# Kernel optimization log

Measured on AMD Instinct MI355X. Metric: run time of the kernel, lower is better.

Reference implementation:

```python
import jax, jax.numpy as jnp
import numpy as np

V, E, H, S = 50257, 1024, 1024, 2048


def setup_inputs() -> dict:
    key = jax.random.key(0)
    ks = jax.random.split(key, 24)
    def n(k, shape, s=0.02):
        return jax.random.normal(k, shape, dtype=jnp.float32) * s
    inp = {
        "x": jax.random.normal(ks[0], (1, E), dtype=jnp.float32),
        "encoder_outputs": jax.random.normal(ks[1], (S, 2 * H), dtype=jnp.float32),
        "sentence": jax.random.randint(ks[2], (S,), 0, V, dtype=jnp.int32).at[0].set(7),
        "prev_probs": jax.random.uniform(ks[3], (V + S,), dtype=jnp.float32),
        "h0": n(ks[4], (1, H), 1.0),
        "c0": n(ks[5], (1, H), 1.0),
        "attn_W": n(ks[6], (S, 2 * H)), "attn_b": jnp.zeros((S,), jnp.float32),
        "comb_W": n(ks[7], (H, 2 * H)), "comb_b": jnp.zeros((H,), jnp.float32),
        "Ws_W": n(ks[8], (H, 2 * H)), "Ws_b": jnp.zeros((H,), jnp.float32),
        "Wo_W": n(ks[9], (V, H)), "Wo_b": jnp.zeros((V,), jnp.float32),
        "Wc_W": n(ks[10], (H, 2 * H)), "Wc_b": jnp.zeros((H,), jnp.float32),
        "W_ih": n(ks[11], (4 * H, E + 2 * H)), "W_hh": n(ks[12], (4 * H, H)),
        "b_ih": jnp.zeros((4 * H,), jnp.float32), "b_hh": jnp.zeros((4 * H,), jnp.float32),
        "prev_word": 7,
    }
    return inp


def reference(x, encoder_outputs, sentence, prev_probs, h0, c0,
              attn_W, attn_b, comb_W, comb_b, Ws_W, Ws_b,
              Wo_W, Wo_b, Wc_W, Wc_b, W_ih, W_hh, b_ih, b_hh, prev_word):
    xe, h, c = x[0], h0[0], c0[0]            # [E], [H], [H]
    # attentive read: attention over encoder positions, then combine to [H]
    att_logits = jnp.concatenate([xe, h]) @ attn_W.T + attn_b      # [S]
    attn_w = jax.nn.softmax(att_logits)
    ctx = attn_w @ encoder_outputs                                 # [2H]
    attentive = ctx @ comb_W.T + comb_b                            # [H]
    # selective read (copy mechanism): positions where sentence == prev_word
    probs_c = prev_probs[V:]                                       # [S]
    rho = jnp.where(sentence == prev_word, probs_c, 0.0)
    rho = rho / (rho.sum() + 1e-9)
    selective = (rho @ encoder_outputs) @ Ws_W.T + Ws_b            # [H]
    # single LSTM step (PyTorch gate order i,f,g,o)
    lstm_in = jnp.concatenate([xe, selective, attentive])          # [E+2H]
    gates = lstm_in @ W_ih.T + b_ih + h @ W_hh.T + b_hh            # [4H]
    i, f, g, o = jnp.split(gates, 4)
    c1 = jax.nn.sigmoid(f) * c + jax.nn.sigmoid(i) * jnp.tanh(g)
    h1 = jax.nn.sigmoid(o) * jnp.tanh(c1)                          # [H]
    # generate + copy scores, joint softmax
    score_g = h1 @ Wo_W.T + Wo_b                                   # [V]
    score_c = jnp.tanh(encoder_outputs @ Wc_W.T + Wc_b) @ h1       # [S]
    probs = jax.nn.softmax(jnp.concatenate([score_g, score_c]))    # [V+S]
    return probs, h1[None, :], c1[None, :]
```

## Files before the change

### kernel.cpp

```cpp
#include <hip/hip_runtime.h>
#include <hip/hip_bf16.h>
#include <math.h>

#define VV 50257
#define EE 1024
#define HH 1024
#define SS 2048
#define VS (VV + SS)

#define OFF_LOGA   0
#define OFF_ATTW   2048
#define OFF_RHO    4096
#define OFF_CTX    6144
#define OFF_SEL    8192
#define OFF_LSTMIN 10240
#define OFF_GATES  13312
#define OFF_H1     17408
#define OFF_LOG    18432
#define OFF_MS     70784
#define OFF_LS     70912
#define OFF_G      71040
#define OFF_TT     71168

typedef __attribute__((ext_vector_type(8))) short bf16x8;
typedef __attribute__((ext_vector_type(4))) float f32x4;

__device__ inline float wave_reduce(float v) {
    #pragma unroll
    for (int off = 32; off > 0; off >>= 1) v += __shfl_down(v, off, 64);
    return v;
}

__device__ inline unsigned short f2bf(float f) {
    unsigned int u = __builtin_bit_cast(unsigned int, f);
    u += 0x7FFFu + ((u >> 16) & 1u);
    return (unsigned short)(u >> 16);
}

__global__ void k_attn_logits(const float* __restrict__ x, const float* __restrict__ h0,
                              const float* __restrict__ attn_W, const float* __restrict__ attn_b,
                              float* __restrict__ out) {
    int wave = (blockIdx.x * blockDim.x + threadIdx.x) >> 6;
    int lane = threadIdx.x & 63;
    if (wave >= SS) return;
    const float4* rp = (const float4*)(attn_W + (size_t)wave * 2048);
    float acc = 0.f;
    #pragma unroll
    for (int k = 0; k < 8; ++k) {
        int idx = lane + 64 * k;
        float4 w = rp[idx];
        int j = idx * 4;
        const float* cat = (j < 1024) ? (x + j) : (h0 + (j - 1024));
        acc += w.x * cat[0] + w.y * cat[1] + w.z * cat[2] + w.w * cat[3];
    }
    acc = wave_reduce(acc);
    if (lane == 0) out[wave] = acc + attn_b[wave];
}

__global__ void k_prep(const float* __restrict__ logits, const int* __restrict__ sentence,
                       const float* __restrict__ prev_probs, const int* __restrict__ prev_word,
                       const float* __restrict__ x,
                       float* __restrict__ attn_w, float* __restrict__ rho,
                       float* __restrict__ lstm_in) {
    __shared__ float red[256];
    int tid = threadIdx.x;
    float m = -1e30f;
    for (int s = tid; s < SS; s += 256) m = fmaxf(m, logits[s]);
    red[tid] = m; __syncthreads();
    for (int o = 128; o > 0; o >>= 1) { if (tid < o) red[tid] = fmaxf(red[tid], red[tid + o]); __syncthreads(); }
    m = red[0]; __syncthreads();
    float sum = 0.f;
    for (int s = tid; s < SS; s += 256) sum += expf(logits[s] - m);
    red[tid] = sum; __syncthreads();
    for (int o = 128; o > 0; o >>= 1) { if (tid < o) red[tid] += red[tid + o]; __syncthreads(); }
    float inv = 1.f / red[0]; __syncthreads();
    for (int s = tid; s < SS; s += 256) attn_w[s] = expf(logits[s] - m) * inv;
    int pw = prev_word[0];
    float rsum = 0.f;
    for (int s = tid; s < SS; s += 256) rsum += (sentence[s] == pw) ? prev_probs[VV + s] : 0.f;
    red[tid] = rsum; __syncthreads();
    for (int o = 128; o > 0; o >>= 1) { if (tid < o) red[tid] += red[tid + o]; __syncthreads(); }
    float rinv = 1.f / (red[0] + 1e-9f); __syncthreads();
    for (int s = tid; s < SS; s += 256) rho[s] = ((sentence[s] == pw) ? prev_probs[VV + s] : 0.f) * rinv;
    for (int j = tid; j < EE; j += 256) lstm_in[j] = x[j];
}

__global__ void k_ctx(const float* __restrict__ enc, const float* __restrict__ attn_w,
                      const float* __restrict__ rho, float* __restrict__ ctx,
                      float* __restrict__ selctx) {
    int col = blockIdx.x * 256 + threadIdx.x;
    int s0 = blockIdx.y * 64;
    float a = 0.f, r = 0.f;
    const float* p = enc + (size_t)s0 * 2048 + col;
    #pragma unroll 4
    for (int i = 0; i < 64; ++i) {
        float v = p[(size_t)i * 2048];
        a += attn_w[s0 + i] * v;
        r += rho[s0 + i] * v;
    }
    atomicAdd(&ctx[col], a);
    atomicAdd(&selctx[col], r);
}

__global__ void k_comb(const float* __restrict__ ctx, const float* __restrict__ selctx,
                       const float* __restrict__ comb_W, const float* __restrict__ comb_b,
                       const float* __restrict__ Ws_W, const float* __restrict__ Ws_b,
                       float* __restrict__ lstm_in) {
    int wave = (blockIdx.x * blockDim.x + threadIdx.x) >> 6;
    int lane = threadIdx.x & 63;
    if (wave >= 2048) return;
    bool sel = wave >= 1024;
    int i = sel ? wave - 1024 : wave;
    const float4* rp = (const float4*)((sel ? Ws_W : comb_W) + (size_t)i * 2048);
    const float4* vp = (const float4*)(sel ? selctx : ctx);
    float acc = 0.f;
    #pragma unroll
    for (int k = 0; k < 8; ++k) {
        int idx = lane + 64 * k;
        float4 w = rp[idx]; float4 v = vp[idx];
        acc += w.x * v.x + w.y * v.y + w.z * v.z + w.w * v.w;
    }
    acc = wave_reduce(acc);
    if (lane == 0) lstm_in[sel ? (1024 + i) : (2048 + i)] = acc + (sel ? Ws_b[i] : comb_b[i]);
}

__global__ void k_gates(const float* __restrict__ lstm_in, const float* __restrict__ h0,
                        const float* __restrict__ W_ih, const float* __restrict__ W_hh,
                        const float* __restrict__ b_ih, const float* __restrict__ b_hh,
                        float* __restrict__ gates) {
    int wave = (blockIdx.x * blockDim.x + threadIdx.x) >> 6;
    int lane = threadIdx.x & 63;
    if (wave >= 4096) return;
    const float4* rp = (const float4*)(W_ih + (size_t)wave * 3072);
    const float4* vp = (const float4*)lstm_in;
    float acc = 0.f;
    #pragma unroll
    for (int k = 0; k < 12; ++k) {
        int idx = lane + 64 * k;
        float4 w = rp[idx]; float4 v = vp[idx];
        acc += w.x * v.x + w.y * v.y + w.z * v.z + w.w * v.w;
    }
    const float4* hp = (const float4*)(W_hh + (size_t)wave * 1024);
    const float4* h4 = (const float4*)h0;
    #pragma unroll
    for (int k = 0; k < 4; ++k) {
        int idx = lane + 64 * k;
        float4 w = hp[idx]; float4 v = h4[idx];
        acc += w.x * v.x + w.y * v.y + w.z * v.z + w.w * v.w;
    }
    acc = wave_reduce(acc);
    if (lane == 0) gates[wave] = acc + b_ih[wave] + b_hh[wave];
}

__global__ void k_lstm(const float* __restrict__ gates, const float* __restrict__ c0,
                       float* __restrict__ out, float* __restrict__ h1ws) {
    int k = blockIdx.x * 256 + threadIdx.x;
    float ig = gates[k], fg = gates[1024 + k], gg = gates[2048 + k], og = gates[3072 + k];
    float si = 1.f / (1.f + expf(-ig));
    float sf = 1.f / (1.f + expf(-fg));
    float so = 1.f / (1.f + expf(-og));
    float c1 = sf * c0[k] + si * tanhf(gg);
    float h1 = so * tanhf(c1);
    out[VS + k] = h1;
    out[VS + 1024 + k] = c1;
    h1ws[k] = h1;
}

__global__ __launch_bounds__(256) void k_wc_gemm(const float* __restrict__ A,
                                                 const float* __restrict__ B,
                                                 const float* __restrict__ bias,
                                                 float* __restrict__ C) {
    __shared__ unsigned short As[128 * 32];
    __shared__ unsigned short Bs[128 * 32];
    int tid = threadIdx.x;
    int mbase = blockIdx.y * 128;
    int nbase = blockIdx.x * 128;
    int lane = tid & 63;
    int wid = tid >> 6;
    int wm = (wid >> 1) * 64;
    int wn = (wid & 1) * 64;
    int lrow = lane & 15;
    int lk = (lane >> 4) * 8;
    f32x4 acc[4][4] = {};
    for (int k0 = 0; k0 < 2048; k0 += 32) {
        #pragma unroll
        for (int i = 0; i < 4; ++i) {
            int fi = tid + 256 * i;
            int row = fi >> 3;
            int kg = fi & 7;
            float4 v = *(const float4*)(A + (size_t)(mbase + row) * 2048 + k0 + kg * 4);
            ushort4 a4 = { f2bf(v.x), f2bf(v.y), f2bf(v.z), f2bf(v.w) };
            *(ushort4*)(As + row * 32 + kg * 4) = a4;
            float4 w = *(const float4*)(B + (size_t)(nbase + row) * 2048 + k0 + kg * 4);
            ushort4 b4 = { f2bf(w.x), f2bf(w.y), f2bf(w.z), f2bf(w.w) };
            *(ushort4*)(Bs + row * 32 + kg * 4) = b4;
        }
        __syncthreads();
        bf16x8 af[4], bfr[4];
        #pragma unroll
        for (int t = 0; t < 4; ++t) {
            af[t]  = *(const bf16x8*)(As + (wm + t * 16 + lrow) * 32 + lk);
            bfr[t] = *(const bf16x8*)(Bs + (wn + t * 16 + lrow) * 32 + lk);
        }
        #pragma unroll
        for (int mt = 0; mt < 4; ++mt)
            #pragma unroll
            for (int nt = 0; nt < 4; ++nt)
                acc[mt][nt] = __builtin_amdgcn_mfma_f32_16x16x32_bf16(af[mt], bfr[nt], acc[mt][nt], 0, 0, 0);
        __syncthreads();
    }
    int crow0 = (lane >> 4) * 4;
    int ccol = lane & 15;
    #pragma unroll
    for (int mt = 0; mt < 4; ++mt)
        #pragma unroll
        for (int nt = 0; nt < 4; ++nt) {
            int col = nbase + wn + nt * 16 + ccol;
            float bb = bias[col];
            #pragma unroll
            for (int r = 0; r < 4; ++r) {
                int row = mbase + wm + mt * 16 + crow0 + r;
                C[(size_t)row * 1024 + col] = tanhf(acc[mt][nt][r] + bb);
            }
        }
}

__global__ void k_scores(const float* __restrict__ Wo_W, const float* __restrict__ Wo_b,
                         const float* __restrict__ Tt, const float* __restrict__ h1,
                         float* __restrict__ logits) {
    int wave = (blockIdx.x * blockDim.x + threadIdx.x) >> 6;
    int lane = threadIdx.x & 63;
    if (wave >= VS) return;
    const float* row = (wave < VV) ? (Wo_W + (size_t)wave * 1024) : (Tt + (size_t)(wave - VV) * 1024);
    const float4* rp = (const float4*)row;
    const float4* hp = (const float4*)h1;
    float acc = 0.f;
    #pragma unroll
    for (int k = 0; k < 4; ++k) {
        int idx = lane + 64 * k;
        float4 w = rp[idx]; float4 v = hp[idx];
        acc += w.x * v.x + w.y * v.y + w.z * v.z + w.w * v.w;
    }
    acc = wave_reduce(acc);
    if (lane == 0) logits[wave] = acc + (wave < VV ? Wo_b[wave] : 0.f);
}

__global__ void k_sm1(const float* __restrict__ logits, float* __restrict__ ms, float* __restrict__ ls) {
    __shared__ float rm[256], rl[256];
    int tid = threadIdx.x;
    float m = -1e30f, l = 0.f;
    for (int v = blockIdx.x * 256 + tid; v < VS; v += 128 * 256) {
        float x = logits[v];
        float nm = fmaxf(m, x);
        l = l * expf(m - nm) + expf(x - nm);
        m = nm;
    }
    rm[tid] = m; rl[tid] = l; __syncthreads();
    for (int o = 128; o > 0; o >>= 1) {
        if (tid < o) {
            float m2 = rm[tid + o], l2 = rl[tid + o];
            float nm = fmaxf(rm[tid], m2);
            rl[tid] = rl[tid] * expf(rm[tid] - nm) + l2 * expf(m2 - nm);
            rm[tid] = nm;
        }
        __syncthreads();
    }
    if (tid == 0) { ms[blockIdx.x] = rm[0]; ls[blockIdx.x] = rl[0]; }
}

__global__ void k_sm2(const float* __restrict__ ms, const float* __restrict__ ls, float* __restrict__ g) {
    __shared__ float rm[128], rl[128];
    int tid = threadIdx.x;
    rm[tid] = ms[tid]; rl[tid] = ls[tid]; __syncthreads();
    for (int o = 64; o > 0; o >>= 1) {
        if (tid < o) {
            float m2 = rm[tid + o], l2 = rl[tid + o];
            float nm = fmaxf(rm[tid], m2);
            rl[tid] = rl[tid] * expf(rm[tid] - nm) + l2 * expf(m2 - nm);
            rm[tid] = nm;
        }
        __syncthreads();
    }
    if (tid == 0) { g[0] = rm[0]; g[1] = 1.f / rl[0]; }
}

__global__ void k_sm3(const float* __restrict__ logits, const float* __restrict__ g,
                      float* __restrict__ out) {
    int v = blockIdx.x * 256 + threadIdx.x;
    if (v < VS) out[v] = expf(logits[v] - g[0]) * g[1];
}

extern "C" void kernel_launch(void* const* d_in, const int* in_sizes, int n_in,
                              void* d_out, int out_size, void* d_ws, size_t ws_size,
                              hipStream_t stream) {
    (void)in_sizes; (void)n_in; (void)out_size; (void)ws_size;
    const float* x          = (const float*)d_in[0];
    const float* enc        = (const float*)d_in[1];
    const int*   sentence   = (const int*)d_in[2];
    const float* prev_probs = (const float*)d_in[3];
    const float* h0         = (const float*)d_in[4];
    const float* c0         = (const float*)d_in[5];
    const float* attn_W     = (const float*)d_in[6];
    const float* attn_b     = (const float*)d_in[7];
    const float* comb_W     = (const float*)d_in[8];
    const float* comb_b     = (const float*)d_in[9];
    const float* Ws_W       = (const float*)d_in[10];
    const float* Ws_b       = (const float*)d_in[11];
    const float* Wo_W       = (const float*)d_in[12];
    const float* Wo_b       = (const float*)d_in[13];
    const float* Wc_W       = (const float*)d_in[14];
    const float* Wc_b       = (const float*)d_in[15];
    const float* W_ih       = (const float*)d_in[16];
    const float* W_hh       = (const float*)d_in[17];
    const float* b_ih       = (const float*)d_in[18];
    const float* b_hh       = (const float*)d_in[19];
    const int*   prev_word  = (const int*)d_in[20];
    float* ws  = (float*)d_ws;
    float* out = (float*)d_out;

    hipMemsetAsync(ws + OFF_CTX, 0, 4096 * sizeof(float), stream);
    k_wc_gemm<<<dim3(8, 16), 256, 0, stream>>>(enc, Wc_W, Wc_b, ws + OFF_TT);
    k_attn_logits<<<512, 256, 0, stream>>>(x, h0, attn_W, attn_b, ws + OFF_LOGA);
    k_prep<<<1, 256, 0, stream>>>(ws + OFF_LOGA, sentence, prev_probs, prev_word, x,
                                  ws + OFF_ATTW, ws + OFF_RHO, ws + OFF_LSTMIN);
    k_ctx<<<dim3(8, 32), 256, 0, stream>>>(enc, ws + OFF_ATTW, ws + OFF_RHO,
                                           ws + OFF_CTX, ws + OFF_SEL);
    k_comb<<<512, 256, 0, stream>>>(ws + OFF_CTX, ws + OFF_SEL, comb_W, comb_b,
                                    Ws_W, Ws_b, ws + OFF_LSTMIN);
    k_gates<<<1024, 256, 0, stream>>>(ws + OFF_LSTMIN, h0, W_ih, W_hh, b_ih, b_hh,
                                      ws + OFF_GATES);
    k_lstm<<<4, 256, 0, stream>>>(ws + OFF_GATES, c0, out, ws + OFF_H1);
    k_scores<<<13077, 256, 0, stream>>>(Wo_W, Wo_b, ws + OFF_TT, ws + OFF_H1, ws + OFF_LOG);
    k_sm1<<<128, 256, 0, stream>>>(ws + OFF_LOG, ws + OFF_MS, ws + OFF_LS);
    k_sm2<<<1, 128, 0, stream>>>(ws + OFF_MS, ws + OFF_LS, ws + OFF_G);
    k_sm3<<<205, 256, 0, stream>>>(ws + OFF_LOG, ws + OFF_G, out);
}
```

Measured before the change: 522.8 us.

## Fuse Wc GEMM into gates kernel with split-K, move tanh into scores

The standalone Wc GEMM (128 blocks) is merged into the gates GEMV launch as 256 extra blocks that compute a split-K (two halves of K) bf16 MFMA GEMM, writing two partial outputs. Bias add and tanh are moved into the copy-score part of k_scores, which reads both partials. The memset is folded into k_prep, and k_ctx now uses float4 loads with fewer blocks. The aim is to fill the GPU better during the bandwidth-bound gates GEMV and drop launches, at the cost of an extra 8MB partial buffer that must be written and read back, and fewer blocks in k_ctx.

```diff
diff --git a/kernel.cpp b/kernel.cpp
--- a/kernel.cpp
+++ b/kernel.cpp
@@ -20,7 +20,8 @@
 #define OFF_MS     70784
 #define OFF_LS     70912
 #define OFF_G      71040
-#define OFF_TT     71168
+#define OFF_T0     71168
+#define OFF_T1     (71168 + 2048*1024)
 
 typedef __attribute__((ext_vector_type(8))) short bf16x8;
 typedef __attribute__((ext_vector_type(4))) float f32x4;
@@ -61,9 +62,10 @@
                        const float* __restrict__ prev_probs, const int* __restrict__ prev_word,
                        const float* __restrict__ x,
                        float* __restrict__ attn_w, float* __restrict__ rho,
-                       float* __restrict__ lstm_in) {
+                       float* __restrict__ lstm_in, float* __restrict__ ctxsel) {
     __shared__ float red[256];
     int tid = threadIdx.x;
+    for (int j = tid; j < 4096; j += 256) ctxsel[j] = 0.f;
     float m = -1e30f;
     for (int s = tid; s < SS; s += 256) m = fmaxf(m, logits[s]);
     red[tid] = m; __syncthreads();
@@ -88,18 +90,20 @@
 __global__ void k_ctx(const float* __restrict__ enc, const float* __restrict__ attn_w,
                       const float* __restrict__ rho, float* __restrict__ ctx,
                       float* __restrict__ selctx) {
-    int col = blockIdx.x * 256 + threadIdx.x;
+    int col4 = blockIdx.x * 256 + threadIdx.x;
     int s0 = blockIdx.y * 64;
-    float a = 0.f, r = 0.f;
-    const float* p = enc + (size_t)s0 * 2048 + col;
+    float4 a = {0.f, 0.f, 0.f, 0.f}, r = {0.f, 0.f, 0.f, 0.f};
+    const float4* p = (const float4*)enc + (size_t)s0 * 512 + col4;
     #pragma unroll 4
     for (int i = 0; i < 64; ++i) {
-        float v = p[(size_t)i * 2048];
-        a += attn_w[s0 + i] * v;
-        r += rho[s0 + i] * v;
-    }
-    atomicAdd(&ctx[col], a);
-    atomicAdd(&selctx[col], r);
+        float4 v = p[(size_t)i * 512];
+        float w = attn_w[s0 + i], q = rho[s0 + i];
+        a.x += w * v.x; a.y += w * v.y; a.z += w * v.z; a.w += w * v.w;
+        r.x += q * v.x; r.y += q * v.y; r.z += q * v.z; r.w += q * v.w;
+    }
+    int c = col4 * 4;
+    atomicAdd(&ctx[c], a.x); atomicAdd(&ctx[c+1], a.y); atomicAdd(&ctx[c+2], a.z); atomicAdd(&ctx[c+3], a.w);
+    atomicAdd(&selctx[c], r.x); atomicAdd(&selctx[c+1], r.y); atomicAdd(&selctx[c+2], r.z); atomicAdd(&selctx[c+3], r.w);
 }
 
 __global__ void k_comb(const float* __restrict__ ctx, const float* __restrict__ selctx,
@@ -124,32 +128,95 @@
     if (lane == 0) lstm_in[sel ? (1024 + i) : (2048 + i)] = acc + (sel ? Ws_b[i] : comb_b[i]);
 }
 
-__global__ void k_gates(const float* __restrict__ lstm_in, const float* __restrict__ h0,
-                        const float* __restrict__ W_ih, const float* __restrict__ W_hh,
-                        const float* __restrict__ b_ih, const float* __restrict__ b_hh,
-                        float* __restrict__ gates) {
-    int wave = (blockIdx.x * blockDim.x + threadIdx.x) >> 6;
-    int lane = threadIdx.x & 63;
-    if (wave >= 4096) return;
-    const float4* rp = (const float4*)(W_ih + (size_t)wave * 3072);
-    const float4* vp = (const float4*)lstm_in;
-    float acc = 0.f;
+__global__ __launch_bounds__(256) void k_gates_gemm(
+        const float* __restrict__ lstm_in, const float* __restrict__ h0,
+        const float* __restrict__ W_ih, const float* __restrict__ W_hh,
+        const float* __restrict__ b_ih, const float* __restrict__ b_hh,
+        float* __restrict__ gates,
+        const float* __restrict__ A,
+        const float* __restrict__ B,
+        float* __restrict__ T0, float* __restrict__ T1) {
+    __shared__ unsigned short As[128 * 32];
+    __shared__ unsigned short Bs[128 * 32];
+    int tid = threadIdx.x;
+    if (blockIdx.x < 1024) {
+        int wave = (blockIdx.x * 256 + tid) >> 6;
+        int lane = tid & 63;
+        const float4* rp = (const float4*)(W_ih + (size_t)wave * 3072);
+        const float4* vp = (const float4*)lstm_in;
+        float acc = 0.f;
+        #pragma unroll
+        for (int k = 0; k < 12; ++k) {
+            int idx = lane + 64 * k;
+            float4 w = rp[idx]; float4 v = vp[idx];
+            acc += w.x * v.x + w.y * v.y + w.z * v.z + w.w * v.w;
+        }
+        const float4* hp = (const float4*)(W_hh + (size_t)wave * 1024);
+        const float4* h4 = (const float4*)h0;
+        #pragma unroll
+        for (int k = 0; k < 4; ++k) {
+            int idx = lane + 64 * k;
+            float4 w = hp[idx]; float4 v = h4[idx];
+            acc += w.x * v.x + w.y * v.y + w.z * v.z + w.w * v.w;
+        }
+        acc = wave_reduce(acc);
+        if (lane == 0) gates[wave] = acc + b_ih[wave] + b_hh[wave];
+        return;
+    }
+    int gg = blockIdx.x - 1024;
+    int sK = gg >> 7;
+    int rem = gg & 127;
+    int mbase = (rem >> 3) * 128;
+    int nbase = (rem & 7) * 128;
+    float* C = sK ? T1 : T0;
+    int lane = tid & 63;
+    int wid = tid >> 6;
+    int wm = (wid >> 1) * 64;
+    int wn = (wid & 1) * 64;
+    int lrow = lane & 15;
+    int lk = (lane >> 4) * 8;
+    f32x4 acc[4][4] = {};
+    int kbeg = sK * 1024;
+    for (int k0 = kbeg; k0 < kbeg + 1024; k0 += 32) {
+        #pragma unroll
+        for (int i = 0; i < 4; ++i) {
+            int fi = tid + 256 * i;
+            int row = fi >> 3;
+            int kg = fi & 7;
+            float4 v = *(const float4*)(A + (size_t)(mbase + row) * 2048 + k0 + kg * 4);
+            ushort4 a4 = { f2bf(v.x), f2bf(v.y), f2bf(v.z), f2bf(v.w) };
+            *(ushort4*)(As + row * 32 + kg * 4) = a4;
+            float4 w = *(const float4*)(B + (size_t)(nbase + row) * 2048 + k0 + kg * 4);
+            ushort4 b4 = { f2bf(w.x), f2bf(w.y), f2bf(w.z), f2bf(w.w) };
+            *(ushort4*)(Bs + row * 32 + kg * 4) = b4;
+        }
+        __syncthreads();
+        bf16x8 af[4], bfr[4];
+        #pragma unroll
+        for (int t = 0; t < 4; ++t) {
+            af[t]  = *(const bf16x8*)(As + (wm + t * 16 + lrow) * 32 + lk);
+            bfr[t] = *(const bf16x8*)(Bs + (wn + t * 16 + lrow) * 32 + lk);
+        }
+        #pragma unroll
+        for (int mt = 0; mt < 4; ++mt)
+            #pragma unroll
+            for (int nt = 0; nt < 4; ++nt)
+                acc[mt][nt] = __builtin_amdgcn_mfma_f32_16x16x32_bf16(af[mt], bfr[nt], acc[mt][nt], 0, 0, 0);
+        __syncthreads();
+    }
+    int crow0 = (lane >> 4) * 4;
+    int ccol = lane & 15;
     #pragma unroll
-    for (int k = 0; k < 12; ++k) {
-        int idx = lane + 64 * k;
-        float4 w = rp[idx]; float4 v = vp[idx];
-        acc += w.x * v.x + w.y * v.y + w.z * v.z + w.w * v.w;
-    }
-    const float4* hp = (const float4*)(W_hh + (size_t)wave * 1024);
-    const float4* h4 = (const float4*)h0;
-    #pragma unroll
-    for (int k = 0; k < 4; ++k) {
-        int idx = lane + 64 * k;
-        float4 w = hp[idx]; float4 v = h4[idx];
-        acc += w.x * v.x + w.y * v.y + w.z * v.z + w.w * v.w;
-    }
-    acc = wave_reduce(acc);
-    if (lane == 0) gates[wave] = acc + b_ih[wave] + b_hh[wave];
+    for (int mt = 0; mt < 4; ++mt)
+        #pragma unroll
+        for (int nt = 0; nt < 4; ++nt) {
+            int col = nbase + wn + nt * 16 + ccol;
+            #pragma unroll
+            for (int r = 0; r < 4; ++r) {
+                int row = mbase + wm + mt * 16 + crow0 + r;
+                C[(size_t)row * 1024 + col] = acc[mt][nt][r];
+            }
+        }
 }
 
 __global__ void k_lstm(const float* __restrict__ gates, const float* __restrict__ c0,
@@ -166,83 +233,40 @@
     h1ws[k] = h1;
 }
 
-__global__ __launch_bounds__(256) void k_wc_gemm(const float* __restrict__ A,
-                                                 const float* __restrict__ B,
-                                                 const float* __restrict__ bias,
-                                                 float* __restrict__ C) {
-    __shared__ unsigned short As[128 * 32];
-    __shared__ unsigned short Bs[128 * 32];
-    int tid = threadIdx.x;
-    int mbase = blockIdx.y * 128;
-    int nbase = blockIdx.x * 128;
-    int lane = tid & 63;
-    int wid = tid >> 6;
-    int wm = (wid >> 1) * 64;
-    int wn = (wid & 1) * 64;
-    int lrow = lane & 15;
-    int lk = (lane >> 4) * 8;
-    f32x4 acc[4][4] = {};
-    for (int k0 = 0; k0 < 2048; k0 += 32) {
-        #pragma unroll
-        for (int i = 0; i < 4; ++i) {
-            int fi = tid + 256 * i;
-            int row = fi >> 3;
-            int kg = fi & 7;
-            float4 v = *(const float4*)(A + (size_t)(mbase + row) * 2048 + k0 + kg * 4);
-            ushort4 a4 = { f2bf(v.x), f2bf(v.y), f2bf(v.z), f2bf(v.w) };
-            *(ushort4*)(As + row * 32 + kg * 4) = a4;
-            float4 w = *(const float4*)(B + (size_t)(nbase + row) * 2048 + k0 + kg * 4);
-            ushort4 b4 = { f2bf(w.x), f2bf(w.y), f2bf(w.z), f2bf(w.w) };
-            *(ushort4*)(Bs + row * 32 + kg * 4) = b4;
-        }
-        __syncthreads();
-        bf16x8 af[4], bfr[4];
-        #pragma unroll
-        for (int t = 0; t < 4; ++t) {
-            af[t]  = *(const bf16x8*)(As + (wm + t * 16 + lrow) * 32 + lk);
-            bfr[t] = *(const bf16x8*)(Bs + (wn + t * 16 + lrow) * 32 + lk);
-        }
-        #pragma unroll
-        for (int mt = 0; mt < 4; ++mt)
-            #pragma unroll
-            for (int nt = 0; nt < 4; ++nt)
-                acc[mt][nt] = __builtin_amdgcn_mfma_f32_16x16x32_bf16(af[mt], bfr[nt], acc[mt][nt], 0, 0, 0);
-        __syncthreads();
-    }
-    int crow0 = (lane >> 4) * 4;
-    int ccol = lane & 15;
-    #pragma unroll
-    for (int mt = 0; mt < 4; ++mt)
-        #pragma unroll
-        for (int nt = 0; nt < 4; ++nt) {
-            int col = nbase + wn + nt * 16 + ccol;
-            float bb = bias[col];
-            #pragma unroll
-            for (int r = 0; r < 4; ++r) {
-                int row = mbase + wm + mt * 16 + crow0 + r;
-                C[(size_t)row * 1024 + col] = tanhf(acc[mt][nt][r] + bb);
-            }
-        }
-}
-
 __global__ void k_scores(const float* __restrict__ Wo_W, const float* __restrict__ Wo_b,
-                         const float* __restrict__ Tt, const float* __restrict__ h1,
-                         float* __restrict__ logits) {
+                         const float* __restrict__ T0, const float* __restrict__ T1,
+                         const float* __restrict__ Wc_b,
+                         const float* __restrict__ h1, float* __restrict__ logits) {
     int wave = (blockIdx.x * blockDim.x + threadIdx.x) >> 6;
     int lane = threadIdx.x & 63;
     if (wave >= VS) return;
-    const float* row = (wave < VV) ? (Wo_W + (size_t)wave * 1024) : (Tt + (size_t)(wave - VV) * 1024);
-    const float4* rp = (const float4*)row;
     const float4* hp = (const float4*)h1;
     float acc = 0.f;
-    #pragma unroll
-    for (int k = 0; k < 4; ++k) {
-        int idx = lane + 64 * k;
-        float4 w = rp[idx]; float4 v = hp[idx];
-        acc += w.x * v.x + w.y * v.y + w.z * v.z + w.w * v.w;
-    }
-    acc = wave_reduce(acc);
-    if (lane == 0) logits[wave] = acc + (wave < VV ? Wo_b[wave] : 0.f);
+    if (wave < VV) {
+        const float4* rp = (const float4*)(Wo_W + (size_t)wave * 1024);
+        #pragma unroll
+        for (int k = 0; k < 4; ++k) {
+            int idx = lane + 64 * k;
+            float4 w = rp[idx]; float4 v = hp[idx];
+            acc += w.x * v.x + w.y * v.y + w.z * v.z + w.w * v.w;
+        }
+        acc = wave_reduce(acc);
+        if (lane == 0) logits[wave] = acc + Wo_b[wave];
+    } else {
+        int r = wave - VV;
+        const float4* p0 = (const float4*)(T0 + (size_t)r * 1024);
+        const float4* p1 = (const float4*)(T1 + (size_t)r * 1024);
+        const float4* bp = (const float4*)Wc_b;
+        #pragma unroll
+        for (int k = 0; k < 4; ++k) {
+            int idx = lane + 64 * k;
+            float4 a0 = p0[idx]; float4 a1 = p1[idx]; float4 bb = bp[idx]; float4 v = hp[idx];
+            acc += tanhf(a0.x + a1.x + bb.x) * v.x + tanhf(a0.y + a1.y + bb.y) * v.y
+                 + tanhf(a0.z + a1.z + bb.z) * v.z + tanhf(a0.w + a1.w + bb.w) * v.w;
+        }
+        acc = wave_reduce(acc);
+        if (lane == 0) logits[wave] = acc;
+    }
 }
 
 __global__ void k_sm1(const float* __restrict__ logits, float* __restrict__ ms, float* __restrict__ ls) {
@@ -318,19 +342,19 @@
     float* ws  = (float*)d_ws;
     float* out = (float*)d_out;
 
-    hipMemsetAsync(ws + OFF_CTX, 0, 4096 * sizeof(float), stream);
-    k_wc_gemm<<<dim3(8, 16), 256, 0, stream>>>(enc, Wc_W, Wc_b, ws + OFF_TT);
     k_attn_logits<<<512, 256, 0, stream>>>(x, h0, attn_W, attn_b, ws + OFF_LOGA);
     k_prep<<<1, 256, 0, stream>>>(ws + OFF_LOGA, sentence, prev_probs, prev_word, x,
-                                  ws + OFF_ATTW, ws + OFF_RHO, ws + OFF_LSTMIN);
-    k_ctx<<<dim3(8, 32), 256, 0, stream>>>(enc, ws + OFF_ATTW, ws + OFF_RHO,
+                                  ws + OFF_ATTW, ws + OFF_RHO, ws + OFF_LSTMIN, ws + OFF_CTX);
+    k_ctx<<<dim3(2, 32), 256, 0, stream>>>(enc, ws + OFF_ATTW, ws + OFF_RHO,
                                            ws + OFF_CTX, ws + OFF_SEL);
     k_comb<<<512, 256, 0, stream>>>(ws + OFF_CTX, ws + OFF_SEL, comb_W, comb_b,
                                     Ws_W, Ws_b, ws + OFF_LSTMIN);
-    k_gates<<<1024, 256, 0, stream>>>(ws + OFF_LSTMIN, h0, W_ih, W_hh, b_ih, b_hh,
-                                      ws + OFF_GATES);
+    k_gates_gemm<<<1280, 256, 0, stream>>>(ws + OFF_LSTMIN, h0, W_ih, W_hh, b_ih, b_hh,
+                                           ws + OFF_GATES, enc, Wc_W,
+                                           ws + OFF_T0, ws + OFF_T1);
     k_lstm<<<4, 256, 0, stream>>>(ws + OFF_GATES, c0, out, ws + OFF_H1);
-    k_scores<<<13077, 256, 0, stream>>>(Wo_W, Wo_b, ws + OFF_TT, ws + OFF_H1, ws + OFF_LOG);
+    k_scores<<<13077, 256, 0, stream>>>(Wo_W, Wo_b, ws + OFF_T0, ws + OFF_T1, Wc_b,
+                                        ws + OFF_H1, ws + OFF_LOG);
     k_sm1<<<128, 256, 0, stream>>>(ws + OFF_LOG, ws + OFF_MS, ws + OFF_LS);
     k_sm2<<<1, 128, 0, stream>>>(ws + OFF_MS, ws + OFF_LS, ws + OFF_G);
     k_sm3<<<205, 256, 0, stream>>>(ws + OFF_LOG, ws + OFF_G, out);
```

Measured after the change: 480.5 us. 1.09x faster.
